# Optimization experiments

Measured on AMD Instinct MI355X. Metric: run time of the kernel, lower is better.

## Reference

```python
import jax, jax.numpy as jnp
import numpy as np

N = 33554432  # 2**25 elements
EPS = 1e-4    # keep probabilities strictly inside (0,1) to avoid log(0)

def setup_inputs() -> dict:
    key = jax.random.key(0)
    k1, k2 = jax.random.split(key)
    input_ = jax.random.uniform(k1, (N,), dtype=jnp.float32, minval=EPS, maxval=1.0 - EPS)
    target = jax.random.uniform(k2, (N,), dtype=jnp.float32, minval=EPS, maxval=1.0 - EPS)
    return {"input": input_, "target": target}

def reference(input, target):
    # Binary KL divergence per element, summed:
    # KL(p||q) = p*log(p/q) + (1-p)*log((1-p)/(1-q))
    p, q = input, target
    kl = p * (jnp.log(p) - jnp.log(q)) + (1.0 - p) * (jnp.log1p(-p) - jnp.log1p(-q))
    return kl.sum()
```

## Files before the change

### kernel.cpp

```cpp
#include <hip/hip_runtime.h>

#define BLOCK  256
#define GRID   2048
#define S4     512
#define STAGES 8

typedef float vfloat4 __attribute__((ext_vector_type(4)));

__device__ __forceinline__ void async_cp16(const vfloat4* g, vfloat4* lds_base) {
    __builtin_amdgcn_global_load_lds(
        (const __attribute__((address_space(1))) unsigned int*)g,
        (__attribute__((address_space(3))) unsigned int*)lds_base,
        16, 0, 0);
}

__device__ __forceinline__ void kl_acc(float p, float q, float& acc) {
    float omp = 1.0f - p;
    float omq = 1.0f - q;
    float d1  = __log2f(p)   - __log2f(q);
    float d2  = __log2f(omp) - __log2f(omq);
    acc = fmaf(p,   d1, acc);
    acc = fmaf(omp, d2, acc);
}

__device__ __forceinline__ void kl_acc4(vfloat4 pv, vfloat4 qv,
                                        float& a0, float& a1, float& a2, float& a3) {
    kl_acc(pv.x, qv.x, a0);
    kl_acc(pv.y, qv.y, a1);
    kl_acc(pv.z, qv.z, a2);
    kl_acc(pv.w, qv.w, a3);
}

__device__ __forceinline__ void block_reduce_and_atomic(float acc, float* out) {
    const float LN2 = 0.69314718055994530942f;
    #pragma unroll
    for (int off = 32; off > 0; off >>= 1)
        acc += __shfl_down(acc, off, 64);

    __shared__ float wave_sums[BLOCK / 64];
    const int lane = threadIdx.x & 63;
    const int wave = threadIdx.x >> 6;
    if (lane == 0) wave_sums[wave] = acc;
    __syncthreads();

    if (threadIdx.x == 0) {
        float s = 0.0f;
        #pragma unroll
        for (int w = 0; w < BLOCK / 64; ++w) s += wave_sums[w];
        atomicAdd(out, s * LN2);
    }
}

__global__ __launch_bounds__(BLOCK, 4) void kl_div_lds(
        const vfloat4* __restrict__ p4,
        const vfloat4* __restrict__ q4,
        float* __restrict__ out) {
    __shared__ vfloat4 sp[2][S4];
    __shared__ vfloat4 sq[2][S4];

    const int t    = threadIdx.x;
    const int w    = t >> 6;
    const int lane = t & 63;
    const size_t base = (size_t)blockIdx.x * (S4 * STAGES);

    auto stage = [&](int s, int buf) {
        const size_t g0 = base + (size_t)s * S4 + w * 128 + lane;
        async_cp16(p4 + g0,      &sp[buf][w * 128]);
        async_cp16(p4 + g0 + 64, &sp[buf][w * 128 + 64]);
        async_cp16(q4 + g0,      &sq[buf][w * 128]);
        async_cp16(q4 + g0 + 64, &sq[buf][w * 128 + 64]);
    };

    stage(0, 0);
    float a0 = 0.0f, a1 = 0.0f, a2 = 0.0f, a3 = 0.0f;

    #pragma unroll
    for (int s = 0; s < STAGES; ++s) {
        const int buf = s & 1;
        __syncthreads();
        if (s + 1 < STAGES) stage(s + 1, buf ^ 1);
        vfloat4 pv0 = sp[buf][t];
        vfloat4 qv0 = sq[buf][t];
        vfloat4 pv1 = sp[buf][t + 256];
        vfloat4 qv1 = sq[buf][t + 256];
        kl_acc4(pv0, qv0, a0, a1, a2, a3);
        kl_acc4(pv1, qv1, a0, a1, a2, a3);
    }

    float acc = (a0 + a1) + (a2 + a3);
    block_reduce_and_atomic(acc, out);
}

__global__ __launch_bounds__(BLOCK) void kl_div_generic(
        const float* __restrict__ p,
        const float* __restrict__ q,
        float* __restrict__ out,
        int n) {
    const int nvec = n >> 2;
    const vfloat4* __restrict__ p4 = reinterpret_cast<const vfloat4*>(p);
    const vfloat4* __restrict__ q4 = reinterpret_cast<const vfloat4*>(q);

    float acc = 0.0f;
    const int stride = gridDim.x * blockDim.x;
    for (int i = blockIdx.x * blockDim.x + threadIdx.x; i < nvec; i += stride) {
        vfloat4 pv = p4[i];
        vfloat4 qv = q4[i];
        kl_acc(pv.x, qv.x, acc);
        kl_acc(pv.y, qv.y, acc);
        kl_acc(pv.z, qv.z, acc);
        kl_acc(pv.w, qv.w, acc);
    }
    for (int i = (nvec << 2) + blockIdx.x * blockDim.x + threadIdx.x; i < n; i += stride) {
        kl_acc(p[i], q[i], acc);
    }
    block_reduce_and_atomic(acc, out);
}

extern "C" void kernel_launch(void* const* d_in, const int* in_sizes, int n_in,
                              void* d_out, int out_size, void* d_ws, size_t ws_size,
                              hipStream_t stream) {
    const float* p = (const float*)d_in[0];
    const float* q = (const float*)d_in[1];
    float* out = (float*)d_out;
    const int n = in_sizes[0];

    hipMemsetAsync(out, 0, sizeof(float), stream);

    if (n == GRID * S4 * STAGES * 4) {
        kl_div_lds<<<GRID, BLOCK, 0, stream>>>(
            reinterpret_cast<const vfloat4*>(p),
            reinterpret_cast<const vfloat4*>(q), out);
    } else {
        kl_div_generic<<<GRID, BLOCK, 0, stream>>>(p, q, out, n);
    }
}
```

Before: 279.6 us.

## Replace block double-buffer with per-wave 4-deep ring and vmcnt waits

Each wave now owns a contiguous chunk and streams it through a private 4-slot LDS ring for p, while q is loaded directly into registers with nontemporal loads. Block-wide __syncthreads are replaced by explicit s_waitcnt vmcnt values, which keeps three stages in flight per wave. The goal is deeper memory-level parallelism without barrier stalls. The hand-tuned waitcnt counts depend on the exact instruction ordering the compiler emits and on how LDS-DMA loads are counted, so an ordering mistake could be a correctness risk.

```diff
diff --git a/kernel.cpp b/kernel.cpp
--- a/kernel.cpp
+++ b/kernel.cpp
@@ -2,8 +2,10 @@
 
 #define BLOCK  256
 #define GRID   2048
-#define S4     512
+#define W4     1024
+#define S4W    128
 #define STAGES 8
+#define RING   4
 
 typedef float vfloat4 __attribute__((ext_vector_type(4)));
 
@@ -51,41 +53,47 @@
     }
 }
 
-__global__ __launch_bounds__(BLOCK, 4) void kl_div_lds(
+__global__ __launch_bounds__(BLOCK, 4) void kl_div_ring(
         const vfloat4* __restrict__ p4,
         const vfloat4* __restrict__ q4,
         float* __restrict__ out) {
-    __shared__ vfloat4 sp[2][S4];
-    __shared__ vfloat4 sq[2][S4];
+    __shared__ vfloat4 sp[4][RING][S4W];
 
     const int t    = threadIdx.x;
     const int w    = t >> 6;
     const int lane = t & 63;
-    const size_t base = (size_t)blockIdx.x * (S4 * STAGES);
+    const size_t wbase = ((size_t)blockIdx.x * 4 + w) * W4;
 
-    auto stage = [&](int s, int buf) {
-        const size_t g0 = base + (size_t)s * S4 + w * 128 + lane;
-        async_cp16(p4 + g0,      &sp[buf][w * 128]);
-        async_cp16(p4 + g0 + 64, &sp[buf][w * 128 + 64]);
-        async_cp16(q4 + g0,      &sq[buf][w * 128]);
-        async_cp16(q4 + g0 + 64, &sq[buf][w * 128 + 64]);
-    };
-
-    stage(0, 0);
+    vfloat4 qr[RING][2];
     float a0 = 0.0f, a1 = 0.0f, a2 = 0.0f, a3 = 0.0f;
 
-    #pragma unroll
-    for (int s = 0; s < STAGES; ++s) {
-        const int buf = s & 1;
-        __syncthreads();
-        if (s + 1 < STAGES) stage(s + 1, buf ^ 1);
-        vfloat4 pv0 = sp[buf][t];
-        vfloat4 qv0 = sq[buf][t];
-        vfloat4 pv1 = sp[buf][t + 256];
-        vfloat4 qv1 = sq[buf][t + 256];
-        kl_acc4(pv0, qv0, a0, a1, a2, a3);
-        kl_acc4(pv1, qv1, a0, a1, a2, a3);
-    }
+    #define ISSUE(S) do {                                                  \
+        const size_t g0 = wbase + (size_t)(S) * S4W + lane;                \
+        vfloat4* dst = &sp[w][(S) & (RING - 1)][0];                        \
+        async_cp16(p4 + g0,      dst);                                     \
+        async_cp16(p4 + g0 + 64, dst + 64);                                \
+        qr[(S) & (RING - 1)][0] = __builtin_nontemporal_load(q4 + g0);     \
+        qr[(S) & (RING - 1)][1] = __builtin_nontemporal_load(q4 + g0 + 64);\
+    } while (0)
+
+    #define STEP(S, VM) do {                                               \
+        if ((S) + 3 < STAGES) ISSUE((S) + 3);                              \
+        __builtin_amdgcn_sched_barrier(0);                                 \
+        __builtin_amdgcn_s_waitcnt((VM) | 0x70 | 0xF00);                   \
+        asm volatile("" ::: "memory");                                     \
+        __builtin_amdgcn_sched_barrier(0);                                 \
+        vfloat4 pv0 = sp[w][(S) & (RING - 1)][lane];                       \
+        vfloat4 pv1 = sp[w][(S) & (RING - 1)][lane + 64];                  \
+        kl_acc4(pv0, qr[(S) & (RING - 1)][0], a0, a1, a2, a3);             \
+        kl_acc4(pv1, qr[(S) & (RING - 1)][1], a0, a1, a2, a3);             \
+    } while (0)
+
+    ISSUE(0); ISSUE(1); ISSUE(2);
+    STEP(0, 12); STEP(1, 12); STEP(2, 12); STEP(3, 12);
+    STEP(4, 12); STEP(5, 8);  STEP(6, 4);  STEP(7, 0);
+
+    #undef STEP
+    #undef ISSUE
 
     float acc = (a0 + a1) + (a2 + a3);
     block_reduce_and_atomic(acc, out);
@@ -126,8 +134,8 @@
 
     hipMemsetAsync(out, 0, sizeof(float), stream);
 
-    if (n == GRID * S4 * STAGES * 4) {
-        kl_div_lds<<<GRID, BLOCK, 0, stream>>>(
+    if (n == GRID * 4 * W4 * 4) {
+        kl_div_ring<<<GRID, BLOCK, 0, stream>>>(
             reinterpret_cast<const vfloat4*>(p),
             reinterpret_cast<const vfloat4*>(q), out);
     } else {
```

Measured after the change: 267.1 us. -4.5%, faster.
